# Performance work log

Hardware: AMD Instinct MI355X
Metric: run time of the kernel (lower is better)

The kernel has to match this reference:

```python
import jax, jax.numpy as jnp
import numpy as np

GROUP_SIZE = 64
NUM_HEADS = 16
NUM_KV_HEADS = 4
ROPE_BASE = 10000.0


def rms_norm(x):
    eps = jnp.asarray(jnp.finfo(x.dtype).eps, x.dtype)
    return x * jax.lax.rsqrt(jnp.mean(x * x, axis=-1, keepdims=True) + eps)


def ternary_weight(w, g=GROUP_SIZE):
    # fake-quant with straight-through estimator, matching torch bf16 cast
    wb = w.astype(jnp.bfloat16)
    wg = wb.reshape(-1, g)
    scale = jnp.clip(jnp.mean(jnp.abs(wg), axis=-1, keepdims=True), 1e-8)
    q = jnp.clip(jnp.round(wg / scale), -1, 1)
    wq = (q * scale).reshape(w.shape)
    return wb + jax.lax.stop_gradient(wq - wb)


def ternary_linear(x, w):
    wt = ternary_weight(w).astype(x.dtype)
    return x @ wt.T


def apply_rotary_emb(x, cos, sin):
    half = x.shape[-1] // 2
    x1, x2 = x[..., :half], x[..., half:]
    return jnp.concatenate((x1 * cos + x2 * sin, x1 * -sin + x2 * cos), axis=-1)


def rotary_tables(seq_len, head_dim, dtype):
    inv_freq = 1.0 / (ROPE_BASE ** (jnp.arange(0, head_dim, 2, dtype=jnp.float32) / head_dim))
    freqs = jnp.outer(jnp.arange(seq_len, dtype=jnp.float32), inv_freq)  # [S, D/2]
    cos = jnp.cos(freqs)[None, :, None, :].astype(dtype)  # [1,S,1,D/2]
    sin = jnp.sin(freqs)[None, :, None, :].astype(dtype)
    return cos, sin


def setup_inputs() -> dict:
    key = jax.random.key(0)
    k1, k2, k3 = jax.random.split(key, 3)
    dim = 1024
    q_size = NUM_HEADS * (dim // NUM_HEADS)
    kv_size = NUM_KV_HEADS * (dim // NUM_HEADS)
    return {
        "x": jax.random.normal(k1, (2, 2048, dim), dtype=jnp.float32),
        "w_qkv": jax.random.normal(k2, (q_size + 2 * kv_size, dim), dtype=jnp.float32) * 0.02,
        "w_proj": jax.random.normal(k3, (dim, dim), dtype=jnp.float32) * 0.02,
        "q_gain": jnp.ones((NUM_HEADS,), dtype=jnp.float32),
    }


def reference(x, w_qkv, w_proj, q_gain):
    bsz, seqlen, dim = x.shape
    head_dim = dim // NUM_HEADS
    q_size = NUM_HEADS * head_dim
    kv_size = NUM_KV_HEADS * head_dim

    qkv = ternary_linear(x, w_qkv)
    q = qkv[..., :q_size].reshape(bsz, seqlen, NUM_HEADS, head_dim)
    k = qkv[..., q_size:q_size + kv_size].reshape(bsz, seqlen, NUM_KV_HEADS, head_dim)
    v = qkv[..., q_size + kv_size:].reshape(bsz, seqlen, NUM_KV_HEADS, head_dim)

    q, k = rms_norm(q), rms_norm(k)
    cos, sin = rotary_tables(seqlen, head_dim, q.dtype)
    q = apply_rotary_emb(q, cos, sin)
    k = apply_rotary_emb(k, cos, sin)
    q = q * q_gain.astype(q.dtype)[None, None, :, None]

    # GQA: repeat kv heads
    rep = NUM_HEADS // NUM_KV_HEADS
    kr = jnp.repeat(k, rep, axis=2)  # [B,S,H,D]
    vr = jnp.repeat(v, rep, axis=2)

    scale = 1.0 / jnp.sqrt(jnp.asarray(head_dim, q.dtype))
    scores = jnp.einsum('bqhd,bkhd->bhqk', q, kr) * scale  # [B,H,S,S]
    causal = jnp.tril(jnp.ones((seqlen, seqlen), dtype=bool))
    scores = jnp.where(causal[None, None], scores, jnp.asarray(-jnp.inf, scores.dtype))
    probs = jax.nn.softmax(scores, axis=-1)
    y = jnp.einsum('bhqk,bkhd->bqhd', probs, vr).reshape(bsz, seqlen, dim)

    # NormedTernaryLinear: rms_norm then ternary linear
    return ternary_linear(rms_norm(y), w_proj)
```

## Files before the change

kernel.cpp:

```cpp
#include <hip/hip_runtime.h>
#include <cstdint>

typedef unsigned short u16;
typedef __bf16 bf16x8 __attribute__((ext_vector_type(8)));
typedef __bf16 bf16x2 __attribute__((ext_vector_type(2)));
typedef short s16x4 __attribute__((ext_vector_type(4)));
typedef int s32x2 __attribute__((ext_vector_type(2)));
typedef float f32x4 __attribute__((ext_vector_type(4)));

__device__ __forceinline__ u16 f2bf(float f) {
    unsigned u = __float_as_uint(f);
    u = (u + 0x7fffu + ((u >> 16) & 1u)) >> 16;
    return (u16)u;
}
__device__ __forceinline__ float bf2f(u16 h) {
    return __uint_as_float(((unsigned)h) << 16);
}

__device__ __forceinline__ void glds16(const u16* g, u16* l) {
    __builtin_amdgcn_global_load_lds(
        (const __attribute__((address_space(1))) void*)g,
        (__attribute__((address_space(3))) void*)l, 16, 0, 0);
}

__device__ __forceinline__ s16x4 pack_bf4(float p0, float p1, float p2, float p3) {
    bf16x2 lo = {(__bf16)p0, (__bf16)p1};
    bf16x2 hi = {(__bf16)p2, (__bf16)p3};
    s32x2 pk = {__builtin_bit_cast(int, lo), __builtin_bit_cast(int, hi)};
    return __builtin_bit_cast(s16x4, pk);
}

#if __has_builtin(__builtin_amdgcn_mfma_f32_16x16x16bf16_1k)
#define MFMA16(a, b, c) __builtin_amdgcn_mfma_f32_16x16x16bf16_1k(a, b, c, 0, 0, 0)
#else
static __device__ __forceinline__ f32x4 mfma16_asm(s16x4 a, s16x4 b, f32x4 c) {
    asm("v_mfma_f32_16x16x16_bf16 %0, %1, %2, %0" : "+v"(c) : "v"(a), "v"(b));
    return c;
}
#define MFMA16(a, b, c) mfma16_asm(a, b, c)
#endif

__global__ __launch_bounds__(256) void prep(
    const float* __restrict__ w_qkv, const float* __restrict__ w_proj,
    const float* __restrict__ x,
    u16* __restrict__ wqkv_b, u16* __restrict__ wproj_b, u16* __restrict__ xb) {
    int bid = blockIdx.x;
    if (bid < 1280) {
        const float* w; u16* o; size_t base;
        if (bid < 768) { w = w_qkv; o = wqkv_b; base = (size_t)bid * 2048; }
        else { w = w_proj; o = wproj_b; base = (size_t)(bid - 768) * 2048; }
        size_t i = base + (size_t)threadIdx.x * 8;
        float4 A = *(const float4*)(w + i);
        float4 B = *(const float4*)(w + i + 4);
        float wf[8] = {A.x, A.y, A.z, A.w, B.x, B.y, B.z, B.w};
        float wbf[8], ab[8];
        #pragma unroll
        for (int e = 0; e < 8; ++e) { wbf[e] = bf2f(f2bf(wf[e])); ab[e] = fabsf(wbf[e]); }
        float s = ((ab[0] + ab[1]) + (ab[2] + ab[3])) + ((ab[4] + ab[5]) + (ab[6] + ab[7]));
        s += __shfl_xor(s, 1);
        s += __shfl_xor(s, 2);
        s += __shfl_xor(s, 4);
        float scale = bf2f(f2bf(s * (1.0f / 64.0f)));
        if (scale < 1e-8f) scale = 1e-8f;
        u16 ov[8];
        #pragma unroll
        for (int e = 0; e < 8; ++e) {
            float t = bf2f(f2bf(wbf[e] / scale));
            float q = rintf(t);
            q = fminf(1.0f, fmaxf(-1.0f, q));
            float d = bf2f(f2bf(q * scale - wbf[e]));
            ov[e] = f2bf(wbf[e] + d);
        }
        *(int4*)(o + i) = *(const int4*)ov;
    } else {
        size_t i = ((size_t)(bid - 1280) * 256 + threadIdx.x) * 8;
        float4 a = *(const float4*)(x + i);
        float4 b = *(const float4*)(x + i + 4);
        u16 o[8] = {f2bf(a.x), f2bf(a.y), f2bf(a.z), f2bf(a.w),
                    f2bf(b.x), f2bf(b.y), f2bf(b.z), f2bf(b.w)};
        *(int4*)(xb + i) = *(const int4*)o;
    }
}

__global__ __launch_bounds__(256) void gemm_qkv(
    const u16* __restrict__ A, const u16* __restrict__ B,
    const float* __restrict__ gain,
    u16* __restrict__ Qb, u16* __restrict__ Kb, u16* __restrict__ Vt) {
    __shared__ u16 As[2][128 * 32];
    __shared__ u16 Bs[2][64 * 32];
    const int tid = threadIdx.x;
    const int lane = tid & 63, w = tid >> 6;
    const int quad = lane >> 4, l16 = lane & 15;
    const int bx = blockIdx.x, by = blockIdx.y;
    const int n0 = bx * 64, t0 = by * 128;
    const bool vblk = bx >= 20;
    const int K = 1024, nk = 32;
    const int b = by >> 4;

    const int sra = w * 16 + (lane >> 2);
    const int srb = tid >> 2;
    const int sg4 = lane & 3;

    f32x4 acc[2][4];
    f32x4 zero = {0.f, 0.f, 0.f, 0.f};
    #pragma unroll
    for (int i = 0; i < 2; ++i)
        #pragma unroll
        for (int j = 0; j < 4; ++j) acc[i][j] = zero;

    int aoff[2], boff[4];
    #pragma unroll
    for (int mi = 0; mi < 2; ++mi) {
        int r = w * 32 + mi * 16 + l16;
        aoff[mi] = r * 32 + (quad ^ ((r >> 1) & 3)) * 8;
    }
    #pragma unroll
    for (int ni = 0; ni < 4; ++ni) {
        int rb = ni * 16 + l16;
        boff[ni] = rb * 32 + (quad ^ ((rb >> 1) & 3)) * 8;
    }

    #pragma unroll
    for (int i = 0; i < 2; ++i) {
        int r = sra + i * 64;
        int g = sg4 ^ ((r >> 1) & 3);
        glds16(A + (size_t)(t0 + r) * K + g * 8, &As[0][0] + (w * 16 + i * 64) * 32 + lane * 8);
    }
    {
        int g = sg4 ^ ((srb >> 1) & 3);
        glds16(B + (size_t)(n0 + srb) * K + g * 8, &Bs[0][0] + w * 512 + lane * 8);
    }
    __syncthreads();

    for (int kt = 0; kt < nk; ++kt) {
        if (kt + 1 < nk) {
            int k0 = (kt + 1) * 32, bi = (kt + 1) & 1;
            #pragma unroll
            for (int i = 0; i < 2; ++i) {
                int r = sra + i * 64;
                int g = sg4 ^ ((r >> 1) & 3);
                glds16(A + (size_t)(t0 + r) * K + k0 + g * 8, &As[bi][0] + (w * 16 + i * 64) * 32 + lane * 8);
            }
            int g = sg4 ^ ((srb >> 1) & 3);
            glds16(B + (size_t)(n0 + srb) * K + k0 + g * 8, &Bs[bi][0] + w * 512 + lane * 8);
        }
        const u16* as = &As[kt & 1][0];
        const u16* bs = &Bs[kt & 1][0];
        bf16x8 af[2], bfr[4];
        #pragma unroll
        for (int mi = 0; mi < 2; ++mi) af[mi]  = *(const bf16x8*)(as + aoff[mi]);
        #pragma unroll
        for (int ni = 0; ni < 4; ++ni) bfr[ni] = *(const bf16x8*)(bs + boff[ni]);
        if (!vblk) {
            #pragma unroll
            for (int mi = 0; mi < 2; ++mi)
                #pragma unroll
                for (int ni = 0; ni < 4; ++ni)
                    acc[mi][ni] = __builtin_amdgcn_mfma_f32_16x16x32_bf16(af[mi], bfr[ni], acc[mi][ni], 0, 0, 0);
        } else {
            #pragma unroll
            for (int mi = 0; mi < 2; ++mi)
                #pragma unroll
                for (int ni = 0; ni < 4; ++ni)
                    acc[mi][ni] = __builtin_amdgcn_mfma_f32_16x16x32_bf16(bfr[ni], af[mi], acc[mi][ni], 0, 0, 0);
        }
        __syncthreads();
    }

    if (vblk) {
        const int kv = bx - 20;
        u16* vbase = Vt + (size_t)(b * 4 + kv) * 64 * 2048;
        const int si = (t0 + w * 32 + l16) & 2047;
        #pragma unroll
        for (int mi = 0; mi < 2; ++mi)
            #pragma unroll
            for (int ni = 0; ni < 4; ++ni) {
                int d = ni * 16 + quad * 4;
                #pragma unroll
                for (int r = 0; r < 4; ++r)
                    vbase[(size_t)(d + r) * 2048 + si + mi * 16] = f2bf(acc[mi][ni][r]);
            }
    } else {
        const bool isQ = bx < 16;
        const float sc = 0.18033688011112042f;
        const float g = isQ ? gain[bx] * sc : 1.0f;
        u16* base = isQ ? (Qb + (size_t)(b * 16 + bx) * 2048 * 64)
                        : (Kb + (size_t)(b * 4 + (bx - 16)) * 2048 * 64);
        const float eps = 1.1920929e-7f;
        const float invf0 = (float)(1.0 / pow(10000.0, (double)l16 / 32.0));
        const float invf1 = (float)(1.0 / pow(10000.0, (double)(l16 + 16) / 32.0));
        #pragma unroll
        for (int mi = 0; mi < 2; ++mi) {
            #pragma unroll
            for (int r = 0; r < 4; ++r) {
                float v0 = acc[mi][0][r], v1 = acc[mi][1][r];
                float v2 = acc[mi][2][r], v3 = acc[mi][3][r];
                float ssq = (v0 * v0 + v1 * v1) + (v2 * v2 + v3 * v3);
                #pragma unroll
                for (int m = 1; m < 16; m <<= 1) ssq += __shfl_xor(ssq, m);
                float rn = 1.0f / sqrtf(ssq * (1.0f / 64.0f) + eps);
                int si = (t0 + w * 32 + mi * 16 + quad * 4 + r) & 2047;
                float a0 = (float)si * invf0, a1 = (float)si * invf1;
                float c0 = __cosf(a0), s0 = __sinf(a0);
                float c1 = __cosf(a1), s1 = __sinf(a1);
                float x1a = v0 * rn, x2a = v2 * rn;
                float x1b = v1 * rn, x2b = v3 * rn;
                u16* row = base + (size_t)si * 64;
                row[l16]      = f2bf((x1a * c0 + x2a * s0) * g);
                row[l16 + 32] = f2bf((x2a * c0 - x1a * s0) * g);
                row[l16 + 16] = f2bf((x1b * c1 + x2b * s1) * g);
                row[l16 + 48] = f2bf((x2b * c1 - x1b * s1) * g);
            }
        }
    }
}

__global__ __launch_bounds__(256) void gemm_bt(
    const u16* __restrict__ A, const u16* __restrict__ B,
    float* __restrict__ C, int M, int N, int K) {
    __shared__ u16 As[2][128 * 32];
    __shared__ u16 Bs[2][64 * 32];
    const int tid = threadIdx.x;
    const int lane = tid & 63, w = tid >> 6;
    const int quad = lane >> 4, l16 = lane & 15;
    const int m0 = blockIdx.y * 128, n0 = blockIdx.x * 64;
    const int wm = (w >> 1) * 64, wn = (w & 1) * 32;

    const int sra = w * 16 + (lane >> 2);
    const int srb = tid >> 2;
    const int sg4 = lane & 3;

    f32x4 acc[4][2];
    f32x4 zero = {0.f, 0.f, 0.f, 0.f};
    #pragma unroll
    for (int i = 0; i < 4; ++i) { acc[i][0] = zero; acc[i][1] = zero; }

    int aoff[4], boff[2];
    #pragma unroll
    for (int mi = 0; mi < 4; ++mi) {
        int r = wm + mi * 16 + l16;
        aoff[mi] = r * 32 + (quad ^ ((r >> 1) & 3)) * 8;
    }
    #pragma unroll
    for (int ni = 0; ni < 2; ++ni) {
        int r = wn + ni * 16 + l16;
        boff[ni] = r * 32 + (quad ^ ((r >> 1) & 3)) * 8;
    }

    const int nk = K >> 5;
    #pragma unroll
    for (int i = 0; i < 2; ++i) {
        int r = sra + i * 64;
        int g = sg4 ^ ((r >> 1) & 3);
        glds16(A + (size_t)(m0 + r) * K + g * 8, &As[0][0] + (w * 16 + i * 64) * 32 + lane * 8);
    }
    {
        int g = sg4 ^ ((srb >> 1) & 3);
        glds16(B + (size_t)(n0 + srb) * K + g * 8, &Bs[0][0] + w * 512 + lane * 8);
    }
    __syncthreads();

    for (int kt = 0; kt < nk; ++kt) {
        if (kt + 1 < nk) {
            int k0 = (kt + 1) * 32, bi = (kt + 1) & 1;
            #pragma unroll
            for (int i = 0; i < 2; ++i) {
                int r = sra + i * 64;
                int g = sg4 ^ ((r >> 1) & 3);
                glds16(A + (size_t)(m0 + r) * K + k0 + g * 8, &As[bi][0] + (w * 16 + i * 64) * 32 + lane * 8);
            }
            int g = sg4 ^ ((srb >> 1) & 3);
            glds16(B + (size_t)(n0 + srb) * K + k0 + g * 8, &Bs[bi][0] + w * 512 + lane * 8);
        }
        const u16* as = &As[kt & 1][0];
        const u16* bs = &Bs[kt & 1][0];
        bf16x8 af[4], bfr[2];
        #pragma unroll
        for (int mi = 0; mi < 4; ++mi) af[mi]  = *(const bf16x8*)(as + aoff[mi]);
        #pragma unroll
        for (int ni = 0; ni < 2; ++ni) bfr[ni] = *(const bf16x8*)(bs + boff[ni]);
        #pragma unroll
        for (int mi = 0; mi < 4; ++mi)
            #pragma unroll
            for (int ni = 0; ni < 2; ++ni)
                acc[mi][ni] = __builtin_amdgcn_mfma_f32_16x16x32_bf16(af[mi], bfr[ni], acc[mi][ni], 0, 0, 0);
        __syncthreads();
    }
    #pragma unroll
    for (int mi = 0; mi < 4; ++mi)
        #pragma unroll
        for (int ni = 0; ni < 2; ++ni) {
            int rg = m0 + wm + mi * 16 + quad * 4;
            int cg = n0 + wn + ni * 16 + l16;
            float* cp = C + (size_t)rg * N + cg;
            #pragma unroll
            for (int r = 0; r < 4; ++r) cp[(size_t)r * N] = acc[mi][ni][r];
        }
}

__global__ __launch_bounds__(256, 4) void attn(
    const u16* __restrict__ Qb, const u16* __restrict__ Kb,
    const u16* __restrict__ Vt, const float* __restrict__ gain,
    float* __restrict__ y, float* __restrict__ Opart, float* __restrict__ ml) {
    __shared__ u16 Ks[2][4096];
    __shared__ u16 Vs[2][4096];
    const int hb = blockIdx.x;
    const int h = hb & 15, b = hb >> 4, kvh = h >> 2;
    const int yid = 39 - blockIdx.y;
    const int nch_t[16] = {1,1,1,1,2,2,2,2,3,3,3,3,4,4,4,4};
    const int cst_t[16] = {0,1,2,3,4,6,8,10,12,15,18,21,24,28,32,36};
    int bq = 0;
    #pragma unroll
    for (int i = 1; i < 16; ++i) if (yid >= cst_t[i]) bq = i;
    const int nc = nch_t[bq], ch = yid - cst_t[bq];
    const int T = 2 * bq + 2;
    const int c0 = ch * T / nc;
    const int nj = (ch + 1) * T / nc - c0;
    const bool partial = nc > 1;
    const int q0 = bq * 128;

    const int tid = threadIdx.x, lane = tid & 63, w = tid >> 6;
    const int quad = lane >> 4, l16 = lane & 15;
    const float nM = -(12.0f * fabsf(gain[h]) + 1.0f);
    const f32x4 minit = {nM, nM, nM, nM};

    const u16* Qg = Qb + ((size_t)(b * 16 + h) * 2048 + q0) * 64;
    const u16* Kg = Kb + (size_t)(b * 4 + kvh) * 2048 * 64;
    const u16* Vg = Vt + (size_t)(b * 4 + kvh) * 64 * 2048;

    const int qr0 = w * 32 + l16;
    const bf16x8 qa00 = *(const bf16x8*)(Qg + (size_t)qr0 * 64 + quad * 8);
    const bf16x8 qa01 = *(const bf16x8*)(Qg + (size_t)qr0 * 64 + 32 + quad * 8);
    const bf16x8 qa10 = *(const bf16x8*)(Qg + (size_t)(qr0 + 16) * 64 + quad * 8);
    const bf16x8 qa11 = *(const bf16x8*)(Qg + (size_t)(qr0 + 16) * 64 + 32 + quad * 8);

    const int sr = tid >> 3;
    const int sg = (tid & 7) ^ (sr & 7);
    const int so = tid * 8;

    {
        int c = (c0 + nj - 1) * 64, bi = (nj - 1) & 1;
        glds16(Kg + (size_t)(c + sr) * 64 + sg * 8,        &Ks[bi][0] + so);
        glds16(Kg + (size_t)(c + sr + 32) * 64 + sg * 8,   &Ks[bi][0] + so + 2048);
        glds16(Vg + (size_t)sr * 2048 + c + sg * 8,        &Vs[bi][0] + so);
        glds16(Vg + (size_t)(sr + 32) * 2048 + c + sg * 8, &Vs[bi][0] + so + 2048);
    }
    __syncthreads();

    f32x4 o0[4], o1[4];
    f32x4 zero = {0.f, 0.f, 0.f, 0.f};
    #pragma unroll
    for (int t = 0; t < 4; ++t) { o0[t] = zero; o1[t] = zero; }
    float l0 = 0.f, l1 = 0.f;

    for (int jj = nj - 1; jj >= 0; --jj) {
        if (jj > 0) {
            int c = (c0 + jj - 1) * 64, bi = (jj - 1) & 1;
            glds16(Kg + (size_t)(c + sr) * 64 + sg * 8,        &Ks[bi][0] + so);
            glds16(Kg + (size_t)(c + sr + 32) * 64 + sg * 8,   &Ks[bi][0] + so + 2048);
            glds16(Vg + (size_t)sr * 2048 + c + sg * 8,        &Vs[bi][0] + so);
            glds16(Vg + (size_t)(sr + 32) * 2048 + c + sg * 8, &Vs[bi][0] + so + 2048);
        }
        const u16* Kt = &Ks[jj & 1][0];
        const u16* Vl = &Vs[jj & 1][0];
        const int jg = c0 + jj;
        const int d0 = 8 * bq + 2 * w - 4 * jg;
        const int d1 = d0 + 1;
        if (d1 >= 0) {
            const int tm0 = d0 < 3 ? d0 : 3;
            const int tm1 = d1 < 3 ? d1 : 3;
            s16x4 pf0[4], pf1[4];
            float rs0 = 0.f, rs1 = 0.f;
            __builtin_amdgcn_s_setprio(1);
            #pragma unroll
            for (int t = 0; t < 4; ++t) {
                if (t <= tm1) {
                    int rk = t * 16 + l16;
                    bf16x8 kb0 = *(const bf16x8*)(Kt + rk * 64 + ((quad ^ (rk & 7)) * 8));
                    bf16x8 kb1 = *(const bf16x8*)(Kt + rk * 64 + (((quad + 4) ^ (rk & 7)) * 8));
                    if (t <= tm0) {
                        f32x4 s = __builtin_amdgcn_mfma_f32_16x16x32_bf16(kb0, qa00, minit, 0, 0, 0);
                        s = __builtin_amdgcn_mfma_f32_16x16x32_bf16(kb1, qa01, s, 0, 0, 0);
                        if (t == d0) {
                            #pragma unroll
                            for (int r = 0; r < 4; ++r)
                                if (quad * 4 + r > l16) s[r] = -1e30f;
                        }
                        float p0 = __builtin_amdgcn_exp2f(s[0]);
                        float p1 = __builtin_amdgcn_exp2f(s[1]);
                        float p2 = __builtin_amdgcn_exp2f(s[2]);
                        float p3 = __builtin_amdgcn_exp2f(s[3]);
                        rs0 += (p0 + p1) + (p2 + p3);
                        pf0[t] = pack_bf4(p0, p1, p2, p3);
                    }
                    {
                        f32x4 s = __builtin_amdgcn_mfma_f32_16x16x32_bf16(kb0, qa10, minit, 0, 0, 0);
                        s = __builtin_amdgcn_mfma_f32_16x16x32_bf16(kb1, qa11, s, 0, 0, 0);
                        if (t == d1) {
                            #pragma unroll
                            for (int r = 0; r < 4; ++r)
                                if (quad * 4 + r > l16) s[r] = -1e30f;
                        }
                        float p0 = __builtin_amdgcn_exp2f(s[0]);
                        float p1 = __builtin_amdgcn_exp2f(s[1]);
                        float p2 = __builtin_amdgcn_exp2f(s[2]);
                        float p3 = __builtin_amdgcn_exp2f(s[3]);
                        rs1 += (p0 + p1) + (p2 + p3);
                        pf1[t] = pack_bf4(p0, p1, p2, p3);
                    }
                }
            }
            l0 += rs0; l1 += rs1;
            #pragma unroll
            for (int dt = 0; dt < 4; ++dt) {
                int rv = dt * 16 + l16;
                #pragma unroll
                for (int kt = 0; kt < 4; ++kt) {
                    if (kt <= tm1) {
                        int gv = 2 * kt + (quad >> 1);
                        s16x4 va = *(const s16x4*)(Vl + rv * 64 + ((gv ^ (rv & 7)) * 8) + (quad & 1) * 4);
                        if (kt <= tm0) o0[dt] = MFMA16(va, pf0[kt], o0[dt]);
                        o1[dt] = MFMA16(va, pf1[kt], o1[dt]);
                    }
                }
            }
            __builtin_amdgcn_s_setprio(0);
        }
        __syncthreads();
    }

    l0 += __shfl_xor(l0, 16);
    l0 += __shfl_xor(l0, 32);
    l1 += __shfl_xor(l1, 16);
    l1 += __shfl_xor(l1, 32);

    const int q = w * 32 + l16;
    if (!partial) {
        const float inv0 = 1.0f / l0, inv1 = 1.0f / l1;
        const size_t row0 = (size_t)b * 2048 + q0 + q;
        #pragma unroll
        for (int dt = 0; dt < 4; ++dt) {
            f32x4 a = o0[dt] * inv0;
            *(f32x4*)(&y[row0 * 1024 + h * 64 + dt * 16 + quad * 4]) = a;
            f32x4 c = o1[dt] * inv1;
            *(f32x4*)(&y[(row0 + 16) * 1024 + h * 64 + dt * 16 + quad * 4]) = c;
        }
    } else {
        const int slot = hb * 36 + (yid - 4);
        float* Op = Opart + (size_t)slot * 8192;
        #pragma unroll
        for (int dt = 0; dt < 4; ++dt) {
            *(f32x4*)(Op + q * 64 + dt * 16 + quad * 4) = o0[dt];
            *(f32x4*)(Op + (q + 16) * 64 + dt * 16 + quad * 4) = o1[dt];
        }
        if (quad == 0) {
            ml[slot * 128 + q] = l0;
            ml[slot * 128 + q + 16] = l1;
        }
    }
}

__global__ __launch_bounds__(256) void rmsnorm_merge(
    const float* __restrict__ y, const float* __restrict__ Opart,
    const float* __restrict__ ml, u16* __restrict__ yb) {
    __shared__ float red[4];
    const int row = blockIdx.x, tid = threadIdx.x;
    const int b = row >> 11, s = row & 2047;
    float4 v;
    if (s < 512) {
        v = *(const float4*)(y + (size_t)row * 1024 + tid * 4);
    } else {
        const int nch_t[16] = {1,1,1,1,2,2,2,2,3,3,3,3,4,4,4,4};
        const int cst_t[16] = {0,1,2,3,4,6,8,10,12,15,18,21,24,28,32,36};
        const int bq = s >> 7, q = s & 127;
        const int e = tid * 4, h = e >> 6, dh = e & 63;
        const int n = nch_t[bq];
        const int slot0 = (b * 16 + h) * 36 + (cst_t[bq] - 4);
        float l = 0.f;
        f32x4 xa = {0.f, 0.f, 0.f, 0.f};
        const float* P = Opart + (size_t)slot0 * 8192 + q * 64 + dh;
        for (int c = 0; c < n; ++c) {
            l += ml[(size_t)(slot0 + c) * 128 + q];
            xa += *(const f32x4*)(P + (size_t)c * 8192);
        }
        float inv = 1.0f / l;
        v.x = xa[0] * inv; v.y = xa[1] * inv; v.z = xa[2] * inv; v.w = xa[3] * inv;
    }
    float ss = v.x * v.x + v.y * v.y + v.z * v.z + v.w * v.w;
    #pragma unroll
    for (int m = 1; m < 64; m <<= 1) ss += __shfl_xor(ss, m);
    if ((tid & 63) == 0) red[tid >> 6] = ss;
    __syncthreads();
    float tot = red[0] + red[1] + red[2] + red[3];
    float rn = 1.0f / sqrtf(tot * (1.0f / 1024.0f) + 1.1920929e-7f);
    u16 o[4] = {f2bf(v.x * rn), f2bf(v.y * rn), f2bf(v.z * rn), f2bf(v.w * rn)};
    *(uint2*)(yb + (size_t)row * 1024 + tid * 4) = *(const uint2*)o;
}

extern "C" void kernel_launch(void* const* d_in, const int* in_sizes, int n_in,
                              void* d_out, int out_size, void* d_ws, size_t ws_size,
                              hipStream_t stream) {
    const float* x      = (const float*)d_in[0];
    const float* w_qkv  = (const float*)d_in[1];
    const float* w_proj = (const float*)d_in[2];
    const float* q_gain = (const float*)d_in[3];
    float* out = (float*)d_out;
    char* ws = (char*)d_ws;

    u16*   wproj_b = (u16*)(ws);
    u16*   xb      = (u16*)(ws + 2097152);
    float* y       = (float*)(ws + 2097152);
    u16*   wqkv_b  = (u16*)(ws + 10485760);
    u16*   Qb      = (u16*)(ws + 18874368);
    u16*   yb      = (u16*)(ws + 18874368);
    u16*   Kb      = (u16*)(ws + 27262976);
    u16*   Vt      = (u16*)(ws + 29360128);
    float* Opart   = (float*)(ws + 31457280);
    float* mlb     = (float*)(ws + 69206016);

    prep<<<3328, 256, 0, stream>>>(w_qkv, w_proj, x, wqkv_b, wproj_b, xb);
    gemm_qkv<<<dim3(24, 32), 256, 0, stream>>>(xb, wqkv_b, q_gain, Qb, Kb, Vt);
    attn<<<dim3(32, 40), 256, 0, stream>>>(Qb, Kb, Vt, q_gain, y, Opart, mlb);
    rmsnorm_merge<<<4096, 256, 0, stream>>>(y, Opart, mlb, yb);
    gemm_bt<<<dim3(16, 32), 256, 0, stream>>>(yb, wproj_b, out, 4096, 1024, 1024);
}
```

Before: 174.9 us.

## Software-pipeline PV matmul one tile behind QK with triple-buffered V

Defers the P·V MFMA for each key tile to the next loop iteration, so it runs alongside the next tile's QK scores and exp. V shared memory becomes triple-buffered so the deferred tile's V stays valid while the next one is prefetched, and a final drain handles the last tile. This aims to hide exp and dependency latency behind matrix work. In exchange it uses 8 KB more LDS and keeps P fragments live across iterations, which raises register pressure under launch_bounds(256,4).

```diff
diff --git a/kernel.cpp b/kernel.cpp
--- a/kernel.cpp
+++ b/kernel.cpp
@@ -303,7 +303,7 @@
     const u16* __restrict__ Vt, const float* __restrict__ gain,
     float* __restrict__ y, float* __restrict__ Opart, float* __restrict__ ml) {
     __shared__ u16 Ks[2][4096];
-    __shared__ u16 Vs[2][4096];
+    __shared__ u16 Vs[3][4096];
     const int hb = blockIdx.x;
     const int h = hb & 15, b = hb >> 4, kvh = h >> 2;
     const int yid = 39 - blockIdx.y;
@@ -339,11 +339,11 @@
     const int so = tid * 8;
 
     {
-        int c = (c0 + nj - 1) * 64, bi = (nj - 1) & 1;
-        glds16(Kg + (size_t)(c + sr) * 64 + sg * 8,        &Ks[bi][0] + so);
-        glds16(Kg + (size_t)(c + sr + 32) * 64 + sg * 8,   &Ks[bi][0] + so + 2048);
-        glds16(Vg + (size_t)sr * 2048 + c + sg * 8,        &Vs[bi][0] + so);
-        glds16(Vg + (size_t)(sr + 32) * 2048 + c + sg * 8, &Vs[bi][0] + so + 2048);
+        int t = nj - 1, c = (c0 + t) * 64;
+        glds16(Kg + (size_t)(c + sr) * 64 + sg * 8,        &Ks[t & 1][0] + so);
+        glds16(Kg + (size_t)(c + sr + 32) * 64 + sg * 8,   &Ks[t & 1][0] + so + 2048);
+        glds16(Vg + (size_t)sr * 2048 + c + sg * 8,        &Vs[t % 3][0] + so);
+        glds16(Vg + (size_t)(sr + 32) * 2048 + c + sg * 8, &Vs[t % 3][0] + so + 2048);
     }
     __syncthreads();
 
@@ -353,25 +353,43 @@
     for (int t = 0; t < 4; ++t) { o0[t] = zero; o1[t] = zero; }
     float l0 = 0.f, l1 = 0.f;
 
+    s16x4 pp0[4], pp1[4];
+    int ptm0 = -1, ptm1 = -1, pvb = 0;
+    bool pend = false;
+
     for (int jj = nj - 1; jj >= 0; --jj) {
         if (jj > 0) {
-            int c = (c0 + jj - 1) * 64, bi = (jj - 1) & 1;
-            glds16(Kg + (size_t)(c + sr) * 64 + sg * 8,        &Ks[bi][0] + so);
-            glds16(Kg + (size_t)(c + sr + 32) * 64 + sg * 8,   &Ks[bi][0] + so + 2048);
-            glds16(Vg + (size_t)sr * 2048 + c + sg * 8,        &Vs[bi][0] + so);
-            glds16(Vg + (size_t)(sr + 32) * 2048 + c + sg * 8, &Vs[bi][0] + so + 2048);
+            int c = (c0 + jj - 1) * 64;
+            glds16(Kg + (size_t)(c + sr) * 64 + sg * 8,        &Ks[(jj - 1) & 1][0] + so);
+            glds16(Kg + (size_t)(c + sr + 32) * 64 + sg * 8,   &Ks[(jj - 1) & 1][0] + so + 2048);
+            glds16(Vg + (size_t)sr * 2048 + c + sg * 8,        &Vs[(jj - 1) % 3][0] + so);
+            glds16(Vg + (size_t)(sr + 32) * 2048 + c + sg * 8, &Vs[(jj - 1) % 3][0] + so + 2048);
+        }
+        __builtin_amdgcn_s_setprio(1);
+        if (pend) {
+            const u16* Vp = &Vs[pvb][0];
+            #pragma unroll
+            for (int dt = 0; dt < 4; ++dt) {
+                int rv = dt * 16 + l16;
+                #pragma unroll
+                for (int kt = 0; kt < 4; ++kt) {
+                    if (kt <= ptm1) {
+                        int gv = 2 * kt + (quad >> 1);
+                        s16x4 va = *(const s16x4*)(Vp + rv * 64 + ((gv ^ (rv & 7)) * 8) + (quad & 1) * 4);
+                        if (kt <= ptm0) o0[dt] = MFMA16(va, pp0[kt], o0[dt]);
+                        o1[dt] = MFMA16(va, pp1[kt], o1[dt]);
+                    }
+                }
+            }
         }
         const u16* Kt = &Ks[jj & 1][0];
-        const u16* Vl = &Vs[jj & 1][0];
         const int jg = c0 + jj;
         const int d0 = 8 * bq + 2 * w - 4 * jg;
         const int d1 = d0 + 1;
         if (d1 >= 0) {
             const int tm0 = d0 < 3 ? d0 : 3;
             const int tm1 = d1 < 3 ? d1 : 3;
-            s16x4 pf0[4], pf1[4];
             float rs0 = 0.f, rs1 = 0.f;
-            __builtin_amdgcn_s_setprio(1);
             #pragma unroll
             for (int t = 0; t < 4; ++t) {
                 if (t <= tm1) {
@@ -391,7 +409,7 @@
                         float p2 = __builtin_amdgcn_exp2f(s[2]);
                         float p3 = __builtin_amdgcn_exp2f(s[3]);
                         rs0 += (p0 + p1) + (p2 + p3);
-                        pf0[t] = pack_bf4(p0, p1, p2, p3);
+                        pp0[t] = pack_bf4(p0, p1, p2, p3);
                     }
                     {
                         f32x4 s = __builtin_amdgcn_mfma_f32_16x16x32_bf16(kb0, qa10, minit, 0, 0, 0);
@@ -406,27 +424,32 @@
                         float p2 = __builtin_amdgcn_exp2f(s[2]);
                         float p3 = __builtin_amdgcn_exp2f(s[3]);
                         rs1 += (p0 + p1) + (p2 + p3);
-                        pf1[t] = pack_bf4(p0, p1, p2, p3);
+                        pp1[t] = pack_bf4(p0, p1, p2, p3);
                     }
                 }
             }
             l0 += rs0; l1 += rs1;
-            #pragma unroll
-            for (int dt = 0; dt < 4; ++dt) {
-                int rv = dt * 16 + l16;
-                #pragma unroll
-                for (int kt = 0; kt < 4; ++kt) {
-                    if (kt <= tm1) {
-                        int gv = 2 * kt + (quad >> 1);
-                        s16x4 va = *(const s16x4*)(Vl + rv * 64 + ((gv ^ (rv & 7)) * 8) + (quad & 1) * 4);
-                        if (kt <= tm0) o0[dt] = MFMA16(va, pf0[kt], o0[dt]);
-                        o1[dt] = MFMA16(va, pf1[kt], o1[dt]);
-                    }
+            ptm0 = tm0; ptm1 = tm1; pvb = jj % 3; pend = true;
+        }
+        __builtin_amdgcn_s_setprio(0);
+        __syncthreads();
+    }
+
+    if (pend) {
+        const u16* Vp = &Vs[pvb][0];
+        #pragma unroll
+        for (int dt = 0; dt < 4; ++dt) {
+            int rv = dt * 16 + l16;
+            #pragma unroll
+            for (int kt = 0; kt < 4; ++kt) {
+                if (kt <= ptm1) {
+                    int gv = 2 * kt + (quad >> 1);
+                    s16x4 va = *(const s16x4*)(Vp + rv * 64 + ((gv ^ (rv & 7)) * 8) + (quad & 1) * 4);
+                    if (kt <= ptm0) o0[dt] = MFMA16(va, pp0[kt], o0[dt]);
+                    o1[dt] = MFMA16(va, pp1[kt], o1[dt]);
                 }
             }
-            __builtin_amdgcn_s_setprio(0);
-        }
-        __syncthreads();
+        }
     }
 
     l0 += __shfl_xor(l0, 16);
```

After: 179.9 us. 1.03x slower.
